# Optimization experiments

Measured on AMD Instinct MI355X. Metric: run time of the kernel, lower is better.

## Reference

```python
import jax, jax.numpy as jnp
import numpy as np
import math

D_MODEL = 1024
D_QUERY = 64

def setup_inputs() -> dict:
    key = jax.random.key(0)
    k1, k2, k3, k4 = jax.random.split(key, 4)
    X = jax.random.normal(k1, (4, 4096, D_MODEL), dtype=jnp.float32)
    # store weights as [in, out] so projection is X @ W (same math as nn.Linear with W^T)
    Wq = jax.random.normal(k2, (D_MODEL, D_QUERY), dtype=jnp.float32) * (1.0 / math.sqrt(D_MODEL))
    Wk = jax.random.normal(k3, (D_MODEL, D_QUERY), dtype=jnp.float32) * (1.0 / math.sqrt(D_MODEL))
    Wv = jax.random.normal(k4, (D_MODEL, D_MODEL), dtype=jnp.float32) * (1.0 / math.sqrt(D_MODEL))
    return {"X": X, "Wq": Wq, "Wk": Wk, "Wv": Wv}

def reference(X, Wq, Wk, Wv):
    B, T, _ = X.shape
    Q = X @ Wq            # [B,T,dq]
    K = X @ Wk            # [B,T,dq]
    V = X @ Wv            # [B,T,d_model]
    scores = jnp.einsum('btd,bsd->bts', Q, K)  # [B,T,T]
    causal = jnp.tril(jnp.ones((T, T), dtype=bool))
    # original masks with -inf BEFORE dividing by sqrt(d_query); -inf/c == -inf so equivalent
    scores = jnp.where(causal[None, :, :], scores, -jnp.inf)
    attn = jax.nn.softmax(scores / math.sqrt(D_QUERY), axis=2)
    return attn @ V       # [B,T,d_model]
```

## Files before the change

kernel.cpp:

```cpp
#include <hip/hip_runtime.h>
#include <stdint.h>

#define DM   1024
#define DQ   64
#define NB   4
#define TT   4096
#define MTOT (NB*TT)

#define QB   64
#define KB   64
#define DVS  256
#define C_EXP 0.18033688011112042f

typedef __attribute__((ext_vector_type(8))) short short8;
typedef __attribute__((ext_vector_type(4))) float f32x4;

__device__ __forceinline__ unsigned short f2bf(float f) {
  union { float f; uint32_t u; } v; v.f = f;
  return (unsigned short)((v.u + 0x7FFFu + ((v.u >> 16) & 1u)) >> 16);
}

__global__ void k_cvt_x(const float* __restrict__ X, unsigned short* __restrict__ Xb) {
  int i = (blockIdx.x * 256 + threadIdx.x) * 4;
  float4 v = *(const float4*)(X + i);
  unsigned short o[4] = {f2bf(v.x), f2bf(v.y), f2bf(v.z), f2bf(v.w)};
  *(uint2*)(Xb + i) = *(uint2*)o;
}

__global__ void k_pack_wqk(const float* __restrict__ Wq, const float* __restrict__ Wk,
                           unsigned short* __restrict__ WqkT) {
  int k = blockIdx.x * 256 + threadIdx.x;
  int n = blockIdx.y;
  float v = (n < DQ) ? Wq[(size_t)k * DQ + n] : Wk[(size_t)k * DQ + (n - DQ)];
  WqkT[(size_t)n * DM + k] = f2bf(v);
}

__global__ void k_pack_wv(const float* __restrict__ Wv, unsigned short* __restrict__ WvT) {
  int k = blockIdx.x * 256 + threadIdx.x;
  int n = blockIdx.y;
  WvT[(size_t)n * DM + k] = f2bf(Wv[(size_t)k * DM + n]);
}

template<bool TSTORE>
__global__ __launch_bounds__(256, 2) void k_gemm(
    const unsigned short* __restrict__ A, const unsigned short* __restrict__ Bt,
    unsigned short* __restrict__ C, int M, int N, int K) {
  __shared__ unsigned short As[128 * 32];
  __shared__ unsigned short Bs[128 * 32];
  int tid = threadIdx.x;
  int lane = tid & 63;
  int w = tid >> 6;
  int lo = lane & 15, hi = lane >> 4;
  int bm = blockIdx.x * 128, bn = blockIdx.y * 128;
  int wr = (w >> 1) * 64, wc = (w & 1) * 64;
  f32x4 acc[4][4] = {};
  int arow = tid >> 2, koff = (tid & 3) * 8;
  const unsigned short* Ag = A  + (size_t)(bm + arow) * K + koff;
  const unsigned short* Bg = Bt + (size_t)(bn + arow) * K + koff;

  for (int kt = 0; kt < K; kt += 32) {
    __builtin_amdgcn_global_load_lds((const __attribute__((address_space(1))) void*)(Ag + kt),
        (__attribute__((address_space(3))) void*)(As + tid * 8), 16, 0, 0);
    __builtin_amdgcn_global_load_lds((const __attribute__((address_space(1))) void*)(Ag + (size_t)64 * K + kt),
        (__attribute__((address_space(3))) void*)(As + 2048 + tid * 8), 16, 0, 0);
    __builtin_amdgcn_global_load_lds((const __attribute__((address_space(1))) void*)(Bg + kt),
        (__attribute__((address_space(3))) void*)(Bs + tid * 8), 16, 0, 0);
    __builtin_amdgcn_global_load_lds((const __attribute__((address_space(1))) void*)(Bg + (size_t)64 * K + kt),
        (__attribute__((address_space(3))) void*)(Bs + 2048 + tid * 8), 16, 0, 0);
    __syncthreads();
    short8 af[4], bfr[4];
#pragma unroll
    for (int i = 0; i < 4; i++)
      af[i] = *(const short8*)(As + (wr + i * 16 + lo) * 32 + hi * 8);
#pragma unroll
    for (int j = 0; j < 4; j++)
      bfr[j] = *(const short8*)(Bs + (wc + j * 16 + lo) * 32 + hi * 8);
#pragma unroll
    for (int i = 0; i < 4; i++)
#pragma unroll
      for (int j = 0; j < 4; j++)
        acc[i][j] = __builtin_amdgcn_mfma_f32_16x16x32_bf16(af[i], bfr[j], acc[i][j], 0, 0, 0);
    __syncthreads();
  }

  if (!TSTORE) {
#pragma unroll
    for (int i = 0; i < 4; i++)
#pragma unroll
      for (int j = 0; j < 4; j++) {
        int r0 = bm + wr + i * 16 + hi * 4;
        int c0 = bn + wc + j * 16 + lo;
#pragma unroll
        for (int r = 0; r < 4; r++)
          C[(size_t)(r0 + r) * N + c0] = f2bf(acc[i][j][r]);
      }
  } else {
#pragma unroll
    for (int i = 0; i < 4; i++)
#pragma unroll
      for (int j = 0; j < 4; j++) {
        int m0 = bm + wr + i * 16 + hi * 4;
        int c0 = bn + wc + j * 16 + lo;
        int bb = m0 >> 12, t0 = m0 & (TT - 1);
        unsigned short o[4];
#pragma unroll
        for (int r = 0; r < 4; r++) o[r] = f2bf(acc[i][j][r]);
        *(uint2*)(C + ((size_t)bb * DM + c0) * TT + t0) = *(uint2*)o;
      }
  }
}

__global__ __launch_bounds__(256, 2) void k_flash(
    const unsigned short* __restrict__ QKb,
    const unsigned short* __restrict__ Vt,
    float* __restrict__ Out) {
  __shared__ unsigned short Ks[KB * 64];
  __shared__ unsigned short Vs[DVS * KB];
  __shared__ unsigned short Ps[4][16 * KB];

  int tid = threadIdx.x, lane = tid & 63, w = tid >> 6;
  int lo = lane & 15, hi = lane >> 4;
  int bx = blockIdx.x;
  int slice = bx & 3;
  int tmp = bx >> 2;
  int pair = tmp & 31;
  int b = tmp >> 5;

  const char* kgb = (const char*)QKb + (size_t)b * TT * 256 + 128;
  const char* vgb = (const char*)Vt + ((size_t)b * DM + (size_t)slice * DVS) * (TT * 2);

  for (int half = 0; half < 2; half++) {
    int qt = half ? (63 - pair) : pair;
    int qg0 = qt * QB + w * 16;
    short8 qf[2];
#pragma unroll
    for (int ks = 0; ks < 2; ks++)
      qf[ks] = *(const short8*)(QKb + ((size_t)b * TT + qg0 + lo) * 128 + ks * 32 + hi * 8);
    f32x4 acc[16];
#pragma unroll
    for (int nt = 0; nt < 16; nt++) acc[nt] = (f32x4){0.f, 0.f, 0.f, 0.f};
    float mrow = -3e38f, lrow = 0.f;
    int nkt = qt + 1;

    for (int kt = 0; kt < nkt; kt++) {
      int kbase = kt * KB;
#pragma unroll
      for (int i = 0; i < 2; i++) {
        int c = tid + i * 256;
        int key = c >> 3;
        int dqb = (c & 7) << 4;
        const char* src = kgb + (size_t)(kbase + key) * 256 + (dqb ^ ((key & 7) << 4));
        __builtin_amdgcn_global_load_lds((const __attribute__((address_space(1))) void*)src,
            (__attribute__((address_space(3))) void*)((char*)Ks + c * 16), 16, 0, 0);
      }
#pragma unroll
      for (int i = 0; i < 8; i++) {
        int c = tid + i * 256;
        int dv = c >> 3;
        int kb2 = (c & 7) << 4;
        const char* src = vgb + (size_t)dv * (TT * 2) + kbase * 2 + (kb2 ^ ((dv & 7) << 4));
        __builtin_amdgcn_global_load_lds((const __attribute__((address_space(1))) void*)src,
            (__attribute__((address_space(3))) void*)((char*)Vs + c * 16), 16, 0, 0);
      }
      __syncthreads();

      if (kbase <= qg0 + 15) {
        f32x4 s[4];
#pragma unroll
        for (int mt = 0; mt < 4; mt++) s[mt] = (f32x4){0.f, 0.f, 0.f, 0.f};
#pragma unroll
        for (int ks = 0; ks < 2; ks++) {
#pragma unroll
          for (int mt = 0; mt < 4; mt++) {
            int key = mt * 16 + lo;
            short8 kf = *(const short8*)((const char*)Ks + key * 128 +
                          ((ks * 64 + hi * 16) ^ ((key & 7) << 4)));
            s[mt] = __builtin_amdgcn_mfma_f32_16x16x32_bf16(kf, qf[ks], s[mt], 0, 0, 0);
          }
        }
        if (kbase + KB - 1 > qg0) {
#pragma unroll
          for (int mt = 0; mt < 4; mt++)
#pragma unroll
            for (int r = 0; r < 4; r++)
              if (kbase + mt * 16 + hi * 4 + r > qg0 + lo) s[mt][r] = -3e38f;
        }
        float mx = -3e38f;
#pragma unroll
        for (int mt = 0; mt < 4; mt++)
#pragma unroll
          for (int r = 0; r < 4; r++) mx = fmaxf(mx, s[mt][r]);
        mx = fmaxf(mx, __shfl_xor(mx, 16));
        mx = fmaxf(mx, __shfl_xor(mx, 32));
        float mnew = fmaxf(mrow, mx);
        float fac = exp2f((mrow - mnew) * C_EXP);
        mrow = mnew;
        float lsum = 0.f;
        char* pw = (char*)Ps[w];
#pragma unroll
        for (int mt = 0; mt < 4; mt++) {
          float p0 = exp2f((s[mt][0] - mnew) * C_EXP);
          float p1 = exp2f((s[mt][1] - mnew) * C_EXP);
          float p2 = exp2f((s[mt][2] - mnew) * C_EXP);
          float p3 = exp2f((s[mt][3] - mnew) * C_EXP);
          lsum += (p0 + p1) + (p2 + p3);
          uint2 pk;
          pk.x = (uint32_t)f2bf(p0) | ((uint32_t)f2bf(p1) << 16);
          pk.y = (uint32_t)f2bf(p2) | ((uint32_t)f2bf(p3) << 16);
          *(uint2*)(pw + lo * 128 + ((mt * 32 + hi * 8) ^ ((lo & 7) << 4))) = pk;
        }
        lsum += __shfl_xor(lsum, 16);
        lsum += __shfl_xor(lsum, 32);
        lrow = lrow * fac + lsum;
        if (__any(fac < 1.f)) {
#pragma unroll
          for (int r = 0; r < 4; r++) {
            float fr = __shfl(fac, hi * 4 + r);
#pragma unroll
            for (int nt = 0; nt < 16; nt++) acc[nt][r] *= fr;
          }
        }
        asm volatile("s_waitcnt lgkmcnt(0)" ::: "memory");
#pragma unroll
        for (int ks = 0; ks < 2; ks++) {
          short8 pf = *(const short8*)(pw + lo * 128 + ((ks * 64 + hi * 16) ^ ((lo & 7) << 4)));
#pragma unroll
          for (int nt = 0; nt < 16; nt++) {
            int dv = nt * 16 + lo;
            short8 vf = *(const short8*)((const char*)Vs + dv * 128 +
                          ((ks * 64 + hi * 16) ^ ((dv & 7) << 4)));
            acc[nt] = __builtin_amdgcn_mfma_f32_16x16x32_bf16(pf, vf, acc[nt], 0, 0, 0);
          }
        }
      }
      __syncthreads();
    }
    float invl = 1.f / lrow;
#pragma unroll
    for (int r = 0; r < 4; r++) {
      float il = __shfl(invl, hi * 4 + r);
      int qrow = qg0 + hi * 4 + r;
      float* op = Out + ((size_t)b * TT + qrow) * DM + (size_t)slice * DVS;
#pragma unroll
      for (int nt = 0; nt < 16; nt++) op[nt * 16 + lo] = acc[nt][r] * il;
    }
  }
}

extern "C" void kernel_launch(void* const* d_in, const int* in_sizes, int n_in,
                              void* d_out, int out_size, void* d_ws, size_t ws_size,
                              hipStream_t stream) {
  const float* X  = (const float*)d_in[0];
  const float* Wq = (const float*)d_in[1];
  const float* Wk = (const float*)d_in[2];
  const float* Wv = (const float*)d_in[3];
  float* Out = (float*)d_out;

  unsigned short* Xb   = (unsigned short*)d_ws;
  unsigned short* QKb  = Xb   + (size_t)MTOT * DM;
  unsigned short* Vt   = QKb  + (size_t)MTOT * 128;
  unsigned short* WqkT = Vt   + (size_t)NB * DM * TT;
  unsigned short* WvT  = WqkT + (size_t)128 * DM;

  k_cvt_x<<<MTOT * DM / 1024, 256, 0, stream>>>(X, Xb);
  k_pack_wqk<<<dim3(DM / 256, 128), 256, 0, stream>>>(Wq, Wk, WqkT);
  k_pack_wv<<<dim3(DM / 256, DM), 256, 0, stream>>>(Wv, WvT);
  k_gemm<false><<<dim3(MTOT / 128, 1), 256, 0, stream>>>(Xb, WqkT, QKb, MTOT, 128, DM);
  k_gemm<true ><<<dim3(MTOT / 128, DM / 128), 256, 0, stream>>>(Xb, WvT, Vt, MTOT, DM, DM);
  k_flash<<<512, 256, 0, stream>>>(QKb, Vt, Out);
}
```

Baseline: 345.5 us.

## Double-buffer GEMM and flash K tiles, stage transposed V store via LDS

The GEMM now double-buffers its LDS tiles, so the next K-slice load is issued before the current slice's MFMAs and one barrier per iteration goes away. The transposed V store is routed through an LDS tile so global writes become 16-byte row-contiguous. In the flash kernel, K tiles are double-buffered and the V load is issued right after the barrier so it overlaps QK^T and softmax. The per-warp skip of fully masked key tiles is removed, so those warps now do extra masked work. The Wv packing uses a shared-memory tiled transpose for coalesced reads and writes.

```diff
diff --git a/kernel.cpp b/kernel.cpp
--- a/kernel.cpp
+++ b/kernel.cpp
@@ -36,17 +36,25 @@
 }
 
 __global__ void k_pack_wv(const float* __restrict__ Wv, unsigned short* __restrict__ WvT) {
-  int k = blockIdx.x * 256 + threadIdx.x;
-  int n = blockIdx.y;
-  WvT[(size_t)n * DM + k] = f2bf(Wv[(size_t)k * DM + n]);
+  __shared__ float t[32][33];
+  int tx = threadIdx.x & 31, ty = threadIdx.x >> 5;
+  int r0 = blockIdx.y * 32, c0 = blockIdx.x * 32;
+#pragma unroll
+  for (int i = 0; i < 4; i++)
+    t[ty + 8 * i][tx] = Wv[(size_t)(r0 + ty + 8 * i) * DM + c0 + tx];
+  __syncthreads();
+#pragma unroll
+  for (int i = 0; i < 4; i++)
+    WvT[(size_t)(c0 + ty + 8 * i) * DM + r0 + tx] = f2bf(t[tx][ty + 8 * i]);
 }
 
 template<bool TSTORE>
 __global__ __launch_bounds__(256, 2) void k_gemm(
     const unsigned short* __restrict__ A, const unsigned short* __restrict__ Bt,
     unsigned short* __restrict__ C, int M, int N, int K) {
-  __shared__ unsigned short As[128 * 32];
-  __shared__ unsigned short Bs[128 * 32];
+  __shared__ __align__(16) char smem[TSTORE ? (128 * 136 * 2) : (4 * 128 * 32 * 2)];
+  unsigned short (*As)[128 * 32] = (unsigned short(*)[128 * 32])smem;
+  unsigned short (*Bs)[128 * 32] = (unsigned short(*)[128 * 32])(smem + 2 * 128 * 32 * 2);
   int tid = threadIdx.x;
   int lane = tid & 63;
   int w = tid >> 6;
@@ -58,32 +66,39 @@
   const unsigned short* Ag = A  + (size_t)(bm + arow) * K + koff;
   const unsigned short* Bg = Bt + (size_t)(bn + arow) * K + koff;
 
-  for (int kt = 0; kt < K; kt += 32) {
-    __builtin_amdgcn_global_load_lds((const __attribute__((address_space(1))) void*)(Ag + kt),
-        (__attribute__((address_space(3))) void*)(As + tid * 8), 16, 0, 0);
-    __builtin_amdgcn_global_load_lds((const __attribute__((address_space(1))) void*)(Ag + (size_t)64 * K + kt),
-        (__attribute__((address_space(3))) void*)(As + 2048 + tid * 8), 16, 0, 0);
-    __builtin_amdgcn_global_load_lds((const __attribute__((address_space(1))) void*)(Bg + kt),
-        (__attribute__((address_space(3))) void*)(Bs + tid * 8), 16, 0, 0);
-    __builtin_amdgcn_global_load_lds((const __attribute__((address_space(1))) void*)(Bg + (size_t)64 * K + kt),
-        (__attribute__((address_space(3))) void*)(Bs + 2048 + tid * 8), 16, 0, 0);
+  auto stage = [&](int ko, int buf) {
+    __builtin_amdgcn_global_load_lds((const __attribute__((address_space(1))) void*)(Ag + ko),
+        (__attribute__((address_space(3))) void*)(As[buf] + tid * 8), 16, 0, 0);
+    __builtin_amdgcn_global_load_lds((const __attribute__((address_space(1))) void*)(Ag + (size_t)64 * K + ko),
+        (__attribute__((address_space(3))) void*)(As[buf] + 2048 + tid * 8), 16, 0, 0);
+    __builtin_amdgcn_global_load_lds((const __attribute__((address_space(1))) void*)(Bg + ko),
+        (__attribute__((address_space(3))) void*)(Bs[buf] + tid * 8), 16, 0, 0);
+    __builtin_amdgcn_global_load_lds((const __attribute__((address_space(1))) void*)(Bg + (size_t)64 * K + ko),
+        (__attribute__((address_space(3))) void*)(Bs[buf] + 2048 + tid * 8), 16, 0, 0);
+  };
+
+  int nkt = K / 32;
+  stage(0, 0);
+  for (int t = 0; t < nkt; t++) {
+    int buf = t & 1;
     __syncthreads();
+    if (t + 1 < nkt) stage((t + 1) * 32, buf ^ 1);
+    __builtin_amdgcn_sched_barrier(0);
     short8 af[4], bfr[4];
 #pragma unroll
     for (int i = 0; i < 4; i++)
-      af[i] = *(const short8*)(As + (wr + i * 16 + lo) * 32 + hi * 8);
+      af[i] = *(const short8*)(As[buf] + (wr + i * 16 + lo) * 32 + hi * 8);
 #pragma unroll
     for (int j = 0; j < 4; j++)
-      bfr[j] = *(const short8*)(Bs + (wc + j * 16 + lo) * 32 + hi * 8);
+      bfr[j] = *(const short8*)(Bs[buf] + (wc + j * 16 + lo) * 32 + hi * 8);
 #pragma unroll
     for (int i = 0; i < 4; i++)
 #pragma unroll
       for (int j = 0; j < 4; j++)
         acc[i][j] = __builtin_amdgcn_mfma_f32_16x16x32_bf16(af[i], bfr[j], acc[i][j], 0, 0, 0);
-    __syncthreads();
   }
 
-  if (!TSTORE) {
+  if constexpr (!TSTORE) {
 #pragma unroll
     for (int i = 0; i < 4; i++)
 #pragma unroll
@@ -95,18 +110,28 @@
           C[(size_t)(r0 + r) * N + c0] = f2bf(acc[i][j][r]);
       }
   } else {
+    unsigned short* Es = (unsigned short*)smem;
+    __syncthreads();
 #pragma unroll
     for (int i = 0; i < 4; i++)
 #pragma unroll
       for (int j = 0; j < 4; j++) {
-        int m0 = bm + wr + i * 16 + hi * 4;
-        int c0 = bn + wc + j * 16 + lo;
-        int bb = m0 >> 12, t0 = m0 & (TT - 1);
+        int nl = wc + j * 16 + lo;
+        int ml = wr + i * 16 + hi * 4;
         unsigned short o[4];
 #pragma unroll
         for (int r = 0; r < 4; r++) o[r] = f2bf(acc[i][j][r]);
-        *(uint2*)(C + ((size_t)bb * DM + c0) * TT + t0) = *(uint2*)o;
-      }
+        *(uint2*)(Es + nl * 136 + ml) = *(uint2*)o;
+      }
+    __syncthreads();
+    int bb = bm >> 12, tbase = bm & (TT - 1);
+#pragma unroll
+    for (int p = 0; p < 8; p++) {
+      int n = (tid >> 4) + p * 16;
+      int mm = (tid & 15) * 8;
+      uint4 v = *(const uint4*)(Es + n * 136 + mm);
+      *(uint4*)(C + ((size_t)bb * DM + bn + n) * TT + tbase + mm) = v;
+    }
   }
 }
 
@@ -114,9 +139,9 @@
     const unsigned short* __restrict__ QKb,
     const unsigned short* __restrict__ Vt,
     float* __restrict__ Out) {
-  __shared__ unsigned short Ks[KB * 64];
-  __shared__ unsigned short Vs[DVS * KB];
-  __shared__ unsigned short Ps[4][16 * KB];
+  __shared__ __align__(16) unsigned short Ks[2][KB * 64];
+  __shared__ __align__(16) unsigned short Vs[DVS * KB];
+  __shared__ __align__(16) unsigned short Ps[4][16 * KB];
 
   int tid = threadIdx.x, lane = tid & 63, w = tid >> 6;
   int lo = lane & 15, hi = lane >> 4;
@@ -128,10 +153,37 @@
 
   const char* kgb = (const char*)QKb + (size_t)b * TT * 256 + 128;
   const char* vgb = (const char*)Vt + ((size_t)b * DM + (size_t)slice * DVS) * (TT * 2);
+  char* pw = (char*)Ps[w];
+
+  auto stageK = [&](int kt, int buf) {
+    int kbase = kt * KB;
+#pragma unroll
+    for (int i = 0; i < 2; i++) {
+      int c = tid + i * 256;
+      int key = c >> 3;
+      int dqb = (c & 7) << 4;
+      const char* src = kgb + (size_t)(kbase + key) * 256 + (dqb ^ ((key & 7) << 4));
+      __builtin_amdgcn_global_load_lds((const __attribute__((address_space(1))) void*)src,
+          (__attribute__((address_space(3))) void*)((char*)Ks[buf] + c * 16), 16, 0, 0);
+    }
+  };
+  auto stageV = [&](int kt) {
+    int kbase = kt * KB;
+#pragma unroll
+    for (int i = 0; i < 8; i++) {
+      int c = tid + i * 256;
+      int dv = c >> 3;
+      int kb2 = (c & 7) << 4;
+      const char* src = vgb + (size_t)dv * (TT * 2) + kbase * 2 + (kb2 ^ ((dv & 7) << 4));
+      __builtin_amdgcn_global_load_lds((const __attribute__((address_space(1))) void*)src,
+          (__attribute__((address_space(3))) void*)((char*)Vs + c * 16), 16, 0, 0);
+    }
+  };
 
   for (int half = 0; half < 2; half++) {
     int qt = half ? (63 - pair) : pair;
     int qg0 = qt * QB + w * 16;
+    int nkt = qt + 1;
     short8 qf[2];
 #pragma unroll
     for (int ks = 0; ks < 2; ks++)
@@ -140,101 +192,88 @@
 #pragma unroll
     for (int nt = 0; nt < 16; nt++) acc[nt] = (f32x4){0.f, 0.f, 0.f, 0.f};
     float mrow = -3e38f, lrow = 0.f;
-    int nkt = qt + 1;
+
+    __syncthreads();
+    stageK(0, 0);
 
     for (int kt = 0; kt < nkt; kt++) {
+      int buf = kt & 1;
       int kbase = kt * KB;
-#pragma unroll
-      for (int i = 0; i < 2; i++) {
-        int c = tid + i * 256;
-        int key = c >> 3;
-        int dqb = (c & 7) << 4;
-        const char* src = kgb + (size_t)(kbase + key) * 256 + (dqb ^ ((key & 7) << 4));
-        __builtin_amdgcn_global_load_lds((const __attribute__((address_space(1))) void*)src,
-            (__attribute__((address_space(3))) void*)((char*)Ks + c * 16), 16, 0, 0);
-      }
-#pragma unroll
-      for (int i = 0; i < 8; i++) {
-        int c = tid + i * 256;
-        int dv = c >> 3;
-        int kb2 = (c & 7) << 4;
-        const char* src = vgb + (size_t)dv * (TT * 2) + kbase * 2 + (kb2 ^ ((dv & 7) << 4));
-        __builtin_amdgcn_global_load_lds((const __attribute__((address_space(1))) void*)src,
-            (__attribute__((address_space(3))) void*)((char*)Vs + c * 16), 16, 0, 0);
-      }
       __syncthreads();
-
-      if (kbase <= qg0 + 15) {
-        f32x4 s[4];
-#pragma unroll
-        for (int mt = 0; mt < 4; mt++) s[mt] = (f32x4){0.f, 0.f, 0.f, 0.f};
-#pragma unroll
-        for (int ks = 0; ks < 2; ks++) {
-#pragma unroll
-          for (int mt = 0; mt < 4; mt++) {
-            int key = mt * 16 + lo;
-            short8 kf = *(const short8*)((const char*)Ks + key * 128 +
-                          ((ks * 64 + hi * 16) ^ ((key & 7) << 4)));
-            s[mt] = __builtin_amdgcn_mfma_f32_16x16x32_bf16(kf, qf[ks], s[mt], 0, 0, 0);
-          }
+      stageV(kt);
+      __builtin_amdgcn_sched_barrier(0);
+
+      f32x4 s[4];
+#pragma unroll
+      for (int mt = 0; mt < 4; mt++) s[mt] = (f32x4){0.f, 0.f, 0.f, 0.f};
+#pragma unroll
+      for (int ks = 0; ks < 2; ks++) {
+#pragma unroll
+        for (int mt = 0; mt < 4; mt++) {
+          int key = mt * 16 + lo;
+          short8 kf = *(const short8*)((const char*)Ks[buf] + key * 128 +
+                        ((ks * 64 + hi * 16) ^ ((key & 7) << 4)));
+          s[mt] = __builtin_amdgcn_mfma_f32_16x16x32_bf16(kf, qf[ks], s[mt], 0, 0, 0);
         }
-        if (kbase + KB - 1 > qg0) {
-#pragma unroll
-          for (int mt = 0; mt < 4; mt++)
-#pragma unroll
-            for (int r = 0; r < 4; r++)
-              if (kbase + mt * 16 + hi * 4 + r > qg0 + lo) s[mt][r] = -3e38f;
+      }
+      if (kbase + KB - 1 > qg0) {
+#pragma unroll
+        for (int mt = 0; mt < 4; mt++)
+#pragma unroll
+          for (int r = 0; r < 4; r++)
+            if (kbase + mt * 16 + hi * 4 + r > qg0 + lo) s[mt][r] = -3e38f;
+      }
+      float mx = -3e38f;
+#pragma unroll
+      for (int mt = 0; mt < 4; mt++)
+        mx = fmaxf(mx, fmaxf(fmaxf(s[mt][0], s[mt][1]), fmaxf(s[mt][2], s[mt][3])));
+      mx = fmaxf(mx, __shfl_xor(mx, 16));
+      mx = fmaxf(mx, __shfl_xor(mx, 32));
+      float mnew = fmaxf(mrow, mx);
+      float fac = exp2f((mrow - mnew) * C_EXP);
+      mrow = mnew;
+      float lsum = 0.f;
+#pragma unroll
+      for (int mt = 0; mt < 4; mt++) {
+        float p0 = exp2f((s[mt][0] - mnew) * C_EXP);
+        float p1 = exp2f((s[mt][1] - mnew) * C_EXP);
+        float p2 = exp2f((s[mt][2] - mnew) * C_EXP);
+        float p3 = exp2f((s[mt][3] - mnew) * C_EXP);
+        lsum += (p0 + p1) + (p2 + p3);
+        uint2 pk;
+        pk.x = (uint32_t)f2bf(p0) | ((uint32_t)f2bf(p1) << 16);
+        pk.y = (uint32_t)f2bf(p2) | ((uint32_t)f2bf(p3) << 16);
+        *(uint2*)(pw + lo * 128 + ((mt * 32 + hi * 8) ^ ((lo & 7) << 4))) = pk;
+      }
+      lsum += __shfl_xor(lsum, 16);
+      lsum += __shfl_xor(lsum, 32);
+      lrow = lrow * fac + lsum;
+      if (__any(fac < 1.f)) {
+#pragma unroll
+        for (int r = 0; r < 4; r++) {
+          float fr = __shfl(fac, hi * 4 + r);
+#pragma unroll
+          for (int nt = 0; nt < 16; nt++) acc[nt][r] *= fr;
         }
-        float mx = -3e38f;
-#pragma unroll
-        for (int mt = 0; mt < 4; mt++)
-#pragma unroll
-          for (int r = 0; r < 4; r++) mx = fmaxf(mx, s[mt][r]);
-        mx = fmaxf(mx, __shfl_xor(mx, 16));
-        mx = fmaxf(mx, __shfl_xor(mx, 32));
-        float mnew = fmaxf(mrow, mx);
-        float fac = exp2f((mrow - mnew) * C_EXP);
-        mrow = mnew;
-        float lsum = 0.f;
-        char* pw = (char*)Ps[w];
-#pragma unroll
-        for (int mt = 0; mt < 4; mt++) {
-          float p0 = exp2f((s[mt][0] - mnew) * C_EXP);
-          float p1 = exp2f((s[mt][1] - mnew) * C_EXP);
-          float p2 = exp2f((s[mt][2] - mnew) * C_EXP);
-          float p3 = exp2f((s[mt][3] - mnew) * C_EXP);
-          lsum += (p0 + p1) + (p2 + p3);
-          uint2 pk;
-          pk.x = (uint32_t)f2bf(p0) | ((uint32_t)f2bf(p1) << 16);
-          pk.y = (uint32_t)f2bf(p2) | ((uint32_t)f2bf(p3) << 16);
-          *(uint2*)(pw + lo * 128 + ((mt * 32 + hi * 8) ^ ((lo & 7) << 4))) = pk;
+      }
+
+      __syncthreads();
+      if (kt + 1 < nkt) stageK(kt + 1, buf ^ 1);
+      __builtin_amdgcn_sched_barrier(0);
+
+#pragma unroll
+      for (int ks = 0; ks < 2; ks++) {
+        short8 pf = *(const short8*)(pw + lo * 128 + ((ks * 64 + hi * 16) ^ ((lo & 7) << 4)));
+#pragma unroll
+        for (int nt = 0; nt < 16; nt++) {
+          int dv = nt * 16 + lo;
+          short8 vf = *(const short8*)((const char*)Vs + dv * 128 +
+                        ((ks * 64 + hi * 16) ^ ((dv & 7) << 4)));
+          acc[nt] = __builtin_amdgcn_mfma_f32_16x16x32_bf16(pf, vf, acc[nt], 0, 0, 0);
         }
-        lsum += __shfl_xor(lsum, 16);
-        lsum += __shfl_xor(lsum, 32);
-        lrow = lrow * fac + lsum;
-        if (__any(fac < 1.f)) {
-#pragma unroll
-          for (int r = 0; r < 4; r++) {
-            float fr = __shfl(fac, hi * 4 + r);
-#pragma unroll
-            for (int nt = 0; nt < 16; nt++) acc[nt][r] *= fr;
-          }
-        }
-        asm volatile("s_waitcnt lgkmcnt(0)" ::: "memory");
-#pragma unroll
-        for (int ks = 0; ks < 2; ks++) {
-          short8 pf = *(const short8*)(pw + lo * 128 + ((ks * 64 + hi * 16) ^ ((lo & 7) << 4)));
-#pragma unroll
-          for (int nt = 0; nt < 16; nt++) {
-            int dv = nt * 16 + lo;
-            short8 vf = *(const short8*)((const char*)Vs + dv * 128 +
-                          ((ks * 64 + hi * 16) ^ ((dv & 7) << 4)));
-            acc[nt] = __builtin_amdgcn_mfma_f32_16x16x32_bf16(pf, vf, acc[nt], 0, 0, 0);
-          }
-        }
-      }
-      __syncthreads();
-    }
+      }
+    }
+
     float invl = 1.f / lrow;
 #pragma unroll
     for (int r = 0; r < 4; r++) {
@@ -264,7 +303,7 @@
 
   k_cvt_x<<<MTOT * DM / 1024, 256, 0, stream>>>(X, Xb);
   k_pack_wqk<<<dim3(DM / 256, 128), 256, 0, stream>>>(Wq, Wk, WqkT);
-  k_pack_wv<<<dim3(DM / 256, DM), 256, 0, stream>>>(Wv, WvT);
+  k_pack_wv<<<dim3(DM / 32, DM / 32), 256, 0, stream>>>(Wv, WvT);
   k_gemm<false><<<dim3(MTOT / 128, 1), 256, 0, stream>>>(Xb, WqkT, QKb, MTOT, 128, DM);
   k_gemm<true ><<<dim3(MTOT / 128, DM / 128), 256, 0, stream>>>(Xb, WvT, Vt, MTOT, DM, DM);
   k_flash<<<512, 256, 0, stream>>>(QKb, Vt, Out);
```

Result: no change. 351.1 us (+1.6%).
